# Performance work log

Measured on AMD Instinct MI355X. Metric: run time of the kernel, lower is better.

## Reference

```python
import jax, jax.numpy as jnp
import numpy as np

# hyperparams matching init_kwargs
T_LEN = 1024
T_LATENCY = 7
TB = T_LATENCY + 1          # t_len_block
N_OUT = 1024
BATCH = 32
FS_SCALE = 10.0             # FastSigmoid default scale


@jax.custom_vjp
def fast_sigmoid(x):
    # forward: Heaviside; backward: fast-sigmoid surrogate
    return (x > 0).astype(x.dtype)

def _fs_fwd(x):
    return (x > 0).astype(x.dtype), x

def _fs_bwd(x, g):
    return (g / (FS_SCALE * jnp.abs(x) + 1.0) ** 2,)

fast_sigmoid.defvjp(_fs_fwd, _fs_bwd)


def setup_inputs() -> dict:
    key = jax.random.key(0)
    k1, k2, k3, k4 = jax.random.split(key, 4)
    x = jax.random.normal(k1, (T_LEN, BATCH, N_OUT), dtype=jnp.float32) * 0.6
    # raw params; forward applies the clamp/abs 'properties' of the module
    beta_raw = jax.random.uniform(k2, (N_OUT,), minval=0.7, maxval=0.99, dtype=jnp.float32)
    p_raw = jax.random.uniform(k3, (N_OUT,), minval=0.5, maxval=0.95, dtype=jnp.float32)
    b_raw = jax.random.uniform(k4, (N_OUT,), minval=0.2, maxval=1.0, dtype=jnp.float32)
    return {"x": x, "beta_raw": beta_raw, "p_raw": p_raw, "b_raw": b_raw}


def reference(x, beta_raw, p_raw, b_raw):
    T, B, N = x.shape
    tb = TB
    n_blocks = T // tb  # t_pad == 0 by construction
    dt = x.dtype

    # clamped properties
    beta = jnp.clip(beta_raw, 0.001, 0.999)          # [N]
    p = jnp.clip(jnp.abs(p_raw), 0.0, 0.999)         # [N]
    bb = jnp.clip(jnp.abs(b_raw), 0.001, 1.0)        # [N]

    t_idx = jnp.arange(tb)
    expo = t_idx[:, None] - t_idx[None, :]            # [tb,tb], t - s
    lower = expo >= 0
    # causal decay kernel: beta^(t-s) for s<=t  (grouped conv1d equivalent)
    beta_pow = jnp.where(lower[:, :, None],
                         beta[None, None, :] ** jnp.maximum(expo, 0)[:, :, None].astype(dt),
                         jnp.zeros((), dt))           # [tb,tb,N]
    # phi kernel: weight (t-s+1) for s<=t  (conv2d equivalent)
    phi = jnp.where(lower, (expo + 1).astype(dt), jnp.zeros((), dt))  # [tb,tb]
    p_exp = jnp.arange(1, tb + 1, dtype=dt)           # [tb]
    p_pow = p[None, :] ** p_exp[:, None]              # [tb,N]
    inv_p = 1.0 / p                                   # [N]

    def body(carry, x_slice):
        spikes, z, int_mem, a_kernel = carry          # [tb,B,N],[tb,B,N],[B,N],[tb,B,N]
        sg = jax.lax.stop_gradient(spikes)            # detach_spike_grad=True
        maskf = (jnp.max(sg, axis=0) > 0).astype(dt)  # [B,N] any spike in prev block
        # refractory masking of input
        xs = jnp.where(z < maskf[None], jnp.zeros((), dt), x_slice)
        v_init = int_mem * (1.0 - maskf)
        # adaptation update
        a_at_spike = jnp.sum(a_kernel * sg, axis=0) + inv_p          # [B,N]
        decay_steps = jnp.sum(z > 1, axis=0).astype(dt)              # [B,N]
        new_a = a_at_spike * jnp.power(p[None, :], decay_steps)
        a = a_kernel[-1] * (1.0 - maskf) + new_a * maskf             # [B,N]
        a_k = p_pow[:, None, :] * a[None]                             # [tb,B,N]
        v_th = 1.0 + bb[None, None, :] * a_k                          # [tb,B,N]
        # --- Block forward ---
        cur = xs.at[0].add(beta[None, :] * v_init)
        membrane = jnp.einsum('tsn,sbn->tbn', beta_pow, cur)          # causal decayed sum
        faulty = fast_sigmoid(membrane - v_th)                        # [tb,B,N] 0/1
        z_new = jnp.einsum('ts,sbn->tbn', phi, faulty)
        # g(): keep only entries exactly 1, straight-through grad
        spikes_new = z_new - jax.lax.stop_gradient(
            jnp.where(z_new == 1.0, jnp.zeros((), dt), z_new))
        return (spikes_new, z_new, membrane[-1], a_k), spikes_new

    z0 = jnp.zeros((tb, B, N), dt)
    carry0 = (z0, z0, jnp.zeros((B, N), dt), z0)
    xb = x.reshape(n_blocks, tb, B, N)
    _, out = jax.lax.scan(body, carry0, xb)
    return out.reshape(T, B, N)
```

## Files before the change

### kernel.cpp

```cpp
#include <hip/hip_runtime.h>


constexpr int T_LEN = 1024;
constexpr int TB    = 8;
constexpr int NBLK  = T_LEN / TB;
constexpr int BATCH = 32;
constexpr int NOUT  = 1024;
constexpr int BN    = BATCH * NOUT;
constexpr int W     = 8;
constexpr int NRND  = NBLK / W;
constexpr int RING  = 16;

__device__ __forceinline__ void dma16(const float* g, float* l) {
    __builtin_amdgcn_global_load_lds(
        (const __attribute__((address_space(1))) void*)g,
        (__attribute__((address_space(3))) void*)l, 16, 0, 0);
}

__global__ __launch_bounds__(512, 4)
void snn_blocks_kernel(const float* __restrict__ x,
                       const float* __restrict__ beta_raw,
                       const float* __restrict__ p_raw,
                       const float* __restrict__ b_raw,
                       float* __restrict__ out)
{
    __shared__ float    stg[W][2][TB * 64];
    __shared__ double   carry_ma[RING][2 * 64];
    __shared__ unsigned carry_pk[RING][64];

    const int tid  = threadIdx.x;
    const int lane = tid & 63;
    const int w    = tid >> 6;
    const int wg0  = blockIdx.x * 64;
    const int gid  = wg0 + lane;
    const int n    = gid & (NOUT - 1);

    double beta = (double)beta_raw[n];
    beta = beta < 0.001 ? 0.001 : (beta > 0.999 ? 0.999 : beta);
    double p = fabs((double)p_raw[n]);
    p = p > 0.999 ? 0.999 : p;
    double bb = fabs((double)b_raw[n]);
    bb = bb < 0.001 ? 0.001 : (bb > 1.0 ? 1.0 : bb);
    const double inv_p = 1.0 / p;

    double ppow[9];
    ppow[0] = 1.0;
#pragma unroll
    for (int i = 1; i <= 8; ++i) ppow[i] = ppow[i - 1] * p;
    double bbp[8];
#pragma unroll
    for (int t = 0; t < 8; ++t) bbp[t] = bb * ppow[t + 1];
    const double pp2 = ppow[2], pp4 = ppow[4], pp8 = ppow[8];

    {
        unsigned* pkflat = &carry_pk[0][0];
        pkflat[tid]       = 0u;
        pkflat[tid + 512] = 0u;
    }

    const float* xb_dma = x + (ptrdiff_t)(lane >> 4) * BN + wg0 + (lane & 15) * 4;
    {
        const float* g = xb_dma + (ptrdiff_t)(w * TB) * BN;
        dma16(g,          &stg[w][0][0]);
        dma16(g + 4 * BN, &stg[w][0][256]);
    }
    __syncthreads();

    float* ob = out + gid;

#pragma unroll 1
    for (int r = 0; r < NRND; ++r) {
        const int k = r * W + w;

        if (r > 0)
            asm volatile("s_waitcnt vmcnt(8)" ::: "memory");

        float cur[8];
#pragma unroll
        for (int t = 0; t < 8; ++t)
            cur[t] = stg[w][r & 1][t * 64 + lane];

        double m, a;
        int maskf, firstp;
        if (k == 0) {
            m = 0.0; a = 0.0; maskf = 0; firstp = 0;
        } else {
            const int slot = k & (RING - 1);
            volatile unsigned* vpk = (volatile unsigned*)&carry_pk[slot][lane];
            unsigned pk;
            do { pk = *vpk; } while ((pk >> 8) != (unsigned)k);
            asm volatile("" ::: "memory");
            maskf  = (pk >> 4) & 1;
            firstp = pk & 7;
            m = carry_ma[slot][2 * lane];
            a = carry_ma[slot][2 * lane + 1];
        }

        __builtin_amdgcn_s_setprio(1);

        double pf1 = p;
        pf1 *= (firstp & 1) ? p   : 1.0;
        pf1 *= (firstp & 2) ? pp2 : 1.0;
        pf1 *= (firstp & 4) ? pp4 : 1.0;
        const int dsteps = firstp ^ 7;
        double pd = (dsteps & 1) ? p : 1.0;
        pd *= (dsteps & 2) ? pp2 : 1.0;
        pd *= (dsteps & 4) ? pp4 : 1.0;
        const double new_a = (a * pf1 + inv_p) * pd;
        double vinit;
        if (maskf) { a = new_a;   vinit = 0.0; }
        else       { a = pp8 * a; vinit = m;   }

        const int zmask = maskf ? ((1 << firstp) - 1) : 0;

        int fbits = 0;
        double mm = vinit;
#pragma unroll
        for (int t = 0; t < 8; ++t) {
            const float xf = ((zmask >> t) & 1) ? 0.0f : cur[t];
            mm = beta * mm + (double)xf;
            const double vth = 1.0 + bbp[t] * a;
            fbits |= (mm - vth > 0.0) ? (1 << t) : 0;
        }
        const int nmaskf  = (fbits != 0) ? 1 : 0;
        const int nfirstp = fbits ? __builtin_ctz(fbits) : 0;

        {
            const int s2 = (k + 1) & (RING - 1);
            carry_ma[s2][2 * lane]     = mm;
            carry_ma[s2][2 * lane + 1] = a;
            asm volatile("s_waitcnt lgkmcnt(0)" ::: "memory");
            carry_pk[s2][lane] =
                ((unsigned)(k + 1) << 8) | (nmaskf << 4) | nfirstp;
        }
        __builtin_amdgcn_s_setprio(0);
        asm volatile("" ::: "memory");

        if (k + W < NBLK) {
            const float* g = xb_dma + (ptrdiff_t)((k + W) * TB) * BN;
            float* l = &stg[w][(r + 1) & 1][0];
            dma16(g,          l);
            dma16(g + 4 * BN, l + 256);
        }
        asm volatile("" ::: "memory");

#pragma unroll
        for (int t = 0; t < 8; ++t) {
            const float sv = (nmaskf && t == nfirstp) ? 1.0f : 0.0f;
            ob[(ptrdiff_t)(k * TB + t) * BN] = sv;
        }
        asm volatile("" ::: "memory");
    }
}

extern "C" void kernel_launch(void* const* d_in, const int* in_sizes, int n_in,
                              void* d_out, int out_size, void* d_ws, size_t ws_size,
                              hipStream_t stream) {
    const float* x        = (const float*)d_in[0];
    const float* beta_raw = (const float*)d_in[1];
    const float* p_raw    = (const float*)d_in[2];
    const float* b_raw    = (const float*)d_in[3];
    float* out            = (float*)d_out;

    dim3 grid(BN / 64);
    dim3 block(512);
    snn_blocks_kernel<<<grid, block, 0, stream>>>(x, beta_raw, p_raw, b_raw, out);
}
```

Before: 237.7 us.

## Process four consecutive time blocks per wave between cross-wave carry handoffs

Each wave now runs the serial recurrence over C=4 consecutive 8-step blocks before passing the carry to the next wave, instead of one block per handoff. This cuts the number of LDS spin-wait handoffs on the serial critical path by a factor of four. Staging changes from double-buffered single blocks to a single buffer of four blocks per wave: the data is copied to registers and the next DMA is issued early. The spin loop also adds s_sleep and reads the carry values inside the loop. The cost is more registers and longer serial work per wave, which can reduce how much the waves overlap.

```diff
diff --git a/kernel.cpp b/kernel.cpp
--- a/kernel.cpp
+++ b/kernel.cpp
@@ -8,8 +8,9 @@
 constexpr int NOUT  = 1024;
 constexpr int BN    = BATCH * NOUT;
 constexpr int W     = 8;
-constexpr int NRND  = NBLK / W;
-constexpr int RING  = 16;
+constexpr int C     = 4;
+constexpr int NSR   = NBLK / (W * C);
+constexpr int CRING = 8;
 
 __device__ __forceinline__ void dma16(const float* g, float* l) {
     __builtin_amdgcn_global_load_lds(
@@ -24,9 +25,9 @@
                        const float* __restrict__ b_raw,
                        float* __restrict__ out)
 {
-    __shared__ float    stg[W][2][TB * 64];
-    __shared__ double   carry_ma[RING][2 * 64];
-    __shared__ unsigned carry_pk[RING][64];
+    __shared__ float    stg[W][C][TB * 64];
+    __shared__ double   carry_ma[CRING][2 * 64];
+    __shared__ unsigned carry_pk[CRING][64];
 
     const int tid  = threadIdx.x;
     const int lane = tid & 63;
@@ -52,102 +53,123 @@
     for (int t = 0; t < 8; ++t) bbp[t] = bb * ppow[t + 1];
     const double pp2 = ppow[2], pp4 = ppow[4], pp8 = ppow[8];
 
-    {
-        unsigned* pkflat = &carry_pk[0][0];
-        pkflat[tid]       = 0u;
-        pkflat[tid + 512] = 0u;
-    }
+    (&carry_pk[0][0])[tid] = 0u;
 
-    const float* xb_dma = x + (ptrdiff_t)(lane >> 4) * BN + wg0 + (lane & 15) * 4;
-    {
-        const float* g = xb_dma + (ptrdiff_t)(w * TB) * BN;
-        dma16(g,          &stg[w][0][0]);
-        dma16(g + 4 * BN, &stg[w][0][256]);
+    const float* xb_dma =
+        x + (ptrdiff_t)(lane >> 4) * BN + wg0 + (lane & 15) * 4;
+#pragma unroll
+    for (int c = 0; c < C; ++c) {
+        const int b = w * C + c;
+        const float* g = xb_dma + (ptrdiff_t)(b * TB) * BN;
+        dma16(g,          &stg[w][c][0]);
+        dma16(g + 4 * BN, &stg[w][c][256]);
     }
     __syncthreads();
 
     float* ob = out + gid;
 
 #pragma unroll 1
-    for (int r = 0; r < NRND; ++r) {
-        const int k = r * W + w;
+    for (int r = 0; r < NSR; ++r) {
+        const int h  = r * W + w;
+        const int b0 = h * C;
 
         if (r > 0)
-            asm volatile("s_waitcnt vmcnt(8)" ::: "memory");
+            asm volatile("s_waitcnt vmcnt(32)" ::: "memory");
 
-        float cur[8];
+        float cur[C][8];
 #pragma unroll
-        for (int t = 0; t < 8; ++t)
-            cur[t] = stg[w][r & 1][t * 64 + lane];
+        for (int c = 0; c < C; ++c)
+#pragma unroll
+            for (int t = 0; t < 8; ++t)
+                cur[c][t] = stg[w][c][t * 64 + lane];
+        asm volatile("s_waitcnt lgkmcnt(0)" ::: "memory");
+
+        if (r + 1 < NSR) {
+#pragma unroll
+            for (int c = 0; c < C; ++c) {
+                const int b = (h + W) * C + c;
+                const float* g = xb_dma + (ptrdiff_t)(b * TB) * BN;
+                dma16(g,          &stg[w][c][0]);
+                dma16(g + 4 * BN, &stg[w][c][256]);
+            }
+        }
 
         double m, a;
         int maskf, firstp;
-        if (k == 0) {
+        if (h == 0) {
             m = 0.0; a = 0.0; maskf = 0; firstp = 0;
         } else {
-            const int slot = k & (RING - 1);
-            volatile unsigned* vpk = (volatile unsigned*)&carry_pk[slot][lane];
+            const int slot = h & (CRING - 1);
+            volatile const unsigned* vpk = &carry_pk[slot][lane];
+            volatile const double*   vma = &carry_ma[slot][2 * lane];
             unsigned pk;
-            do { pk = *vpk; } while ((pk >> 8) != (unsigned)k);
+            for (;;) {
+                pk = *vpk;
+                m  = vma[0];
+                a  = vma[1];
+                if ((pk >> 8) == (unsigned)h) break;
+                __builtin_amdgcn_s_sleep(1);
+            }
             asm volatile("" ::: "memory");
             maskf  = (pk >> 4) & 1;
             firstp = pk & 7;
-            m = carry_ma[slot][2 * lane];
-            a = carry_ma[slot][2 * lane + 1];
         }
 
         __builtin_amdgcn_s_setprio(1);
 
-        double pf1 = p;
-        pf1 *= (firstp & 1) ? p   : 1.0;
-        pf1 *= (firstp & 2) ? pp2 : 1.0;
-        pf1 *= (firstp & 4) ? pp4 : 1.0;
-        const int dsteps = firstp ^ 7;
-        double pd = (dsteps & 1) ? p : 1.0;
-        pd *= (dsteps & 2) ? pp2 : 1.0;
-        pd *= (dsteps & 4) ? pp4 : 1.0;
-        const double new_a = (a * pf1 + inv_p) * pd;
-        double vinit;
-        if (maskf) { a = new_a;   vinit = 0.0; }
-        else       { a = pp8 * a; vinit = m;   }
+        int fmk[C], ffp[C];
+#pragma unroll
+        for (int c = 0; c < C; ++c) {
+            double pf1 = p;
+            pf1 *= (firstp & 1) ? p   : 1.0;
+            pf1 *= (firstp & 2) ? pp2 : 1.0;
+            pf1 *= (firstp & 4) ? pp4 : 1.0;
+            const int dsteps = firstp ^ 7;
+            double pd = (dsteps & 1) ? p : 1.0;
+            pd *= (dsteps & 2) ? pp2 : 1.0;
+            pd *= (dsteps & 4) ? pp4 : 1.0;
+            const double new_a = (a * pf1 + inv_p) * pd;
+            double vinit;
+            if (maskf) { a = new_a;   vinit = 0.0; }
+            else       { a = pp8 * a; vinit = m;   }
 
-        const int zmask = maskf ? ((1 << firstp) - 1) : 0;
+            const int zmask = maskf ? ((1 << firstp) - 1) : 0;
 
-        int fbits = 0;
-        double mm = vinit;
+            int fbits = 0;
+            double mm = vinit;
 #pragma unroll
-        for (int t = 0; t < 8; ++t) {
-            const float xf = ((zmask >> t) & 1) ? 0.0f : cur[t];
-            mm = beta * mm + (double)xf;
-            const double vth = 1.0 + bbp[t] * a;
-            fbits |= (mm - vth > 0.0) ? (1 << t) : 0;
+            for (int t = 0; t < 8; ++t) {
+                const float xf = ((zmask >> t) & 1) ? 0.0f : cur[c][t];
+                mm = beta * mm + (double)xf;
+                const double vth = 1.0 + bbp[t] * a;
+                fbits |= (mm - vth > 0.0) ? (1 << t) : 0;
+            }
+            m = mm;
+            maskf  = (fbits != 0) ? 1 : 0;
+            firstp = fbits ? __builtin_ctz(fbits) : 0;
+            fmk[c] = maskf;
+            ffp[c] = firstp;
         }
-        const int nmaskf  = (fbits != 0) ? 1 : 0;
-        const int nfirstp = fbits ? __builtin_ctz(fbits) : 0;
 
         {
-            const int s2 = (k + 1) & (RING - 1);
-            carry_ma[s2][2 * lane]     = mm;
+            const int s2 = (h + 1) & (CRING - 1);
+            carry_ma[s2][2 * lane]     = m;
             carry_ma[s2][2 * lane + 1] = a;
             asm volatile("s_waitcnt lgkmcnt(0)" ::: "memory");
             carry_pk[s2][lane] =
-                ((unsigned)(k + 1) << 8) | (nmaskf << 4) | nfirstp;
+                ((unsigned)(h + 1) << 8) | (maskf << 4) | firstp;
         }
         __builtin_amdgcn_s_setprio(0);
         asm volatile("" ::: "memory");
 
-        if (k + W < NBLK) {
-            const float* g = xb_dma + (ptrdiff_t)((k + W) * TB) * BN;
-            float* l = &stg[w][(r + 1) & 1][0];
-            dma16(g,          l);
-            dma16(g + 4 * BN, l + 256);
-        }
-        asm volatile("" ::: "memory");
-
 #pragma unroll
-        for (int t = 0; t < 8; ++t) {
-            const float sv = (nmaskf && t == nfirstp) ? 1.0f : 0.0f;
-            ob[(ptrdiff_t)(k * TB + t) * BN] = sv;
+        for (int c = 0; c < C; ++c) {
+            const int b = b0 + c;
+#pragma unroll
+            for (int t = 0; t < 8; ++t) {
+                const float sv = (fmk[c] && t == ffp[c]) ? 1.0f : 0.0f;
+                ob[(ptrdiff_t)(b * TB + t) * BN] = sv;
+            }
         }
         asm volatile("" ::: "memory");
     }
```

Result: slower. 255.9 us (+7.6%).
